# Kernel optimization log

Hardware: AMD Instinct MI355X
Metric: run time of the kernel (lower is better)

Reference implementation:

```python
import jax, jax.numpy as jnp
import numpy as np

NLAT = 192  # octahedral O96-class grid


def _lons(nlat):
    half = [20 + 4 * i for i in range(nlat // 2)]
    return half + half[::-1]


def _dft_matrix(nlat, mmax):
    # Truncated per-ring real-DFT basis (torch.fft.rfft convention, 'forward' 1/n norm).
    # Ring j has nlon_j points; frequencies beyond its Nyquist (m > nlon_j//2) are zero.
    lons = _lons(nlat)
    max_nlon = max(lons)
    D = np.zeros((nlat, max_nlon, mmax), dtype=np.complex64)
    for j, n in enumerate(lons):
        keep = min(mmax, n // 2 + 1)
        k = np.arange(n)[:, None]
        m = np.arange(keep)[None, :]
        D[j, :n, :keep] = np.exp(-2j * np.pi * k * m / n) / n
    return D


def _legendre_weights(nlat, lmax, mmax):
    # Orthonormalized associated Legendre P_l^m at Gaussian latitudes (north->south),
    # with Gaussian quadrature weights and the 2*pi longitude factor folded in.
    xg, wg = np.polynomial.legendre.leggauss(nlat)
    x = xg[::-1].copy()
    w = wg[::-1].copy()
    s = np.sqrt(1.0 - x * x)
    leg = np.zeros((lmax, mmax, nlat))
    pmm = np.full(nlat, 1.0 / np.sqrt(4.0 * np.pi))
    for m in range(mmax):
        if m > 0:
            pmm = -np.sqrt((2 * m + 1) / (2.0 * m)) * s * pmm
        if m < lmax:
            leg[m, m] = pmm
        if m + 1 < lmax:
            leg[m + 1, m] = np.sqrt(2 * m + 3.0) * x * pmm
        for l in range(m + 2, lmax):
            a = np.sqrt((4.0 * l * l - 1.0) / (l * l - m * m))
            bb = np.sqrt(((2.0 * l + 1.0) * (l - 1 + m) * (l - 1 - m)) / ((2.0 * l - 3.0) * (l * l - m * m)))
            leg[l, m] = a * x * leg[l - 1, m] - bb * leg[l - 2, m]
    leg = 2.0 * np.pi * leg * w[None, None, :]
    return leg.astype(np.float32)


def setup_inputs() -> dict:
    key = jax.random.key(0)
    nlat = NLAT
    lmax = mmax = nlat // 2
    n_points = sum(_lons(nlat))  # 40320 for nlat=192
    data = jax.random.normal(key, (4, 1, 1, n_points, 100), dtype=jnp.float32)
    dft = jnp.asarray(_dft_matrix(nlat, mmax))
    leg = jnp.asarray(_legendre_weights(nlat, lmax, mmax))
    return {"data": data, "dft": dft, "leg": leg}


def reference(data, dft, leg):
    b, t, e, p, v = data.shape
    nlat, max_nlon, mmax = dft.shape
    lmax = leg.shape[0]
    lons = _lons(nlat)
    # static scatter map: flattened ragged rings -> [nlat, max_nlon] padded layout
    flat_idx = np.concatenate([j * max_nlon + np.arange(n) for j, n in enumerate(lons)])
    x = jnp.transpose(data, (0, 1, 2, 4, 3)).reshape(-1, p)  # [(b t e v), p]
    B = x.shape[0]
    x_pad = jnp.zeros((B, nlat * max_nlon), x.dtype).at[:, flat_idx].set(x)
    x_pad = x_pad.reshape(B, nlat, max_nlon)
    # ragged per-ring truncated real DFT, then associated-Legendre contraction
    f_hat = jnp.einsum('bjn,jnm->bjm', x_pad, dft)        # [B, nlat, mmax] complex
    coeffs = jnp.einsum('bjm,lmj->blm', f_hat, leg)       # [B, lmax, mmax] complex
    coeffs = coeffs.reshape(b, t, e, v, lmax, mmax)
    return jnp.transpose(coeffs, (0, 1, 2, 4, 5, 3))      # [b, t, e, yF, xF, v]
```

## Files before the change

kernel.cpp:

```cpp
#include <hip/hip_runtime.h>

#define NLAT 192
#define NPTS 40320
#define MMAX 96
#define LMAX 96
#define NV   100
#define MAXN 400
#define NB   400

typedef __attribute__((ext_vector_type(8))) _Float16 half8v;
typedef __attribute__((ext_vector_type(4))) float f32x4;

static __device__ __forceinline__ float bits2f(unsigned int b) {
    union { unsigned int i; float f; } v; v.i = b; return v.f;
}
static __device__ __forceinline__ unsigned int f2bf(float f) {
    union { float f; unsigned int i; } v; v.f = f;
    return (v.i + 0x7FFFu + ((v.i >> 16) & 1u)) >> 16;
}
static __device__ __forceinline__ unsigned short f2h(float f) {
    union { _Float16 h; unsigned short s; } u; u.h = (_Float16)f; return u.s;
}
static __device__ __forceinline__ float h2f(unsigned short s) {
    union { _Float16 h; unsigned short s; } u; u.s = s; return (float)u.h;
}
static __device__ __forceinline__ void split2(float a, float b,
                                              unsigned int& hw, unsigned int& lw) {
    unsigned short h0 = f2h(a), h1 = f2h(b);
    unsigned short l0 = f2h(a - h2f(h0)), l1 = f2h(b - h2f(h1));
    hw = (unsigned int)h0 | ((unsigned int)h1 << 16);
    lw = (unsigned int)l0 | ((unsigned int)l1 << 16);
}

static __device__ __forceinline__ int Ssum(int n) {
    int q = n >> 3, r = n & 7; return 4 * q * (q - 1) + q * r;
}
static __device__ __forceinline__ int atoffk(int j) {
    if (j < 96) return 32 * (Ssum(j + 12) - 4);
    return 32 * (672 + 676 - Ssum(204 - j));
}
static __device__ __forceinline__ int kpad_of(int j) {
    return 32 * ((j < 96 ? (j + 12) : (203 - j)) >> 3);
}

__global__ __launch_bounds__(256) void leg_conv_kernel(
    const float* __restrict__ leg,
    unsigned short* __restrict__ legh,
    unsigned short* __restrict__ legl)
{
    int idx = blockIdx.x * 256 + threadIdx.x;
    if (idx >= 96 * 96 * 192) return;
    int j = idx % 192;
    int lm = idx / 192;
    int m = lm % 96, l = lm / 96;
    float v = leg[idx];
    unsigned short h = f2h(v);
    unsigned short lo = f2h(v - h2f(h));
    size_t o = ((size_t)m * 96 + l) * 192 + j;
    legh[o] = h;
    legl[o] = lo;
}

__global__ __launch_bounds__(256) void dft_transpose_kernel(
    const unsigned int* __restrict__ dftw,
    unsigned short* __restrict__ At)
{
    const int j = blockIdx.x;
    const int kpad = kpad_of(j);
    const int t = blockIdx.y;
    const int k0 = t * 32;
    if (k0 >= kpad) return;
    const int n = j < 96 ? 20 + 4 * j : 400 - 4 * (j - 96);
    unsigned short* abase = At + (size_t)atoffk(j) * 192 + (size_t)t * 6144;
    const int tid = threadIdx.x;
#pragma unroll
    for (int s = 0; s < 3; ++s) {
        int slot = s * 256 + tid;
        int row = slot % 192;
        int ch  = slot / 192;
        int m = row < 96 ? row : row - 96;
        bool isIm = row >= 96;
        const unsigned int* dp = dftw + ((size_t)j * MAXN + k0 + ch * 8) * 96 + m;
        unsigned short o[8];
#pragma unroll
        for (int i = 0; i < 8; ++i) {
            int k = k0 + ch * 8 + i;
            unsigned int v = (k < n) ? dp[(size_t)i * 96] : 0u;
            float f = isIm ? bits2f(v & 0xFFFF0000u) : bits2f(v << 16);
            o[i] = f2h(f);
        }
        uint4 pk;
        pk.x = (unsigned int)o[0] | ((unsigned int)o[1] << 16);
        pk.y = (unsigned int)o[2] | ((unsigned int)o[3] << 16);
        pk.z = (unsigned int)o[4] | ((unsigned int)o[5] << 16);
        pk.w = (unsigned int)o[6] | ((unsigned int)o[7] << 16);
        *(uint4*)(abase + (size_t)row * 32 + ch * 8) = pk;
    }
}

__global__ __launch_bounds__(256) void dft_mfma_kernel(
    const float* __restrict__ data,
    const unsigned short* __restrict__ At,
    unsigned short* __restrict__ fh,
    int c0, int cn)
{
    const int id  = blockIdx.x;
    const int j   = id % 192;
    const int bt  = id / 192;
    const int tid = threadIdx.x;
    const int w   = tid >> 6;
    const int l   = tid & 63;
    const int lr  = l & 15;
    const int kg  = l >> 4;

    int n, start;
    if (j < 96) { n = 20 + 4 * j; start = 2 * j * j + 18 * j; }
    else { int jj = j - 96; n = 400 - 4 * jj; start = 20160 + 402 * jj - 2 * jj * jj; }
    const int nsteps = kpad_of(j) >> 5;
    const half8v* avbase = (const half8v*)(At + (size_t)atoffk(j) * 192);

    const int Bb = c0 + bt * 50;
    const int bb = Bb / NV;
    const int vb = Bb % NV;
    const float* dbase = data + (size_t)bb * NPTS * NV + vb;

    f32x4 acc[3][4];
#pragma unroll
    for (int i = 0; i < 3; ++i)
#pragma unroll
        for (int nt = 0; nt < 4; ++nt) acc[i][nt] = (f32x4){0.f, 0.f, 0.f, 0.f};

    float xf[4][8];
#pragma unroll
    for (int nt = 0; nt < 4; ++nt) {
        int c = nt * 16 + lr;
        const float* sp = dbase + (size_t)(start + kg * 8) * NV + c;
#pragma unroll
        for (int i = 0; i < 8; ++i) {
            int k = kg * 8 + i;
            xf[nt][i] = (c < 50 && k < n) ? sp[(size_t)i * NV] : 0.f;
        }
    }

    for (int t = 0; t < nsteps; ++t) {
        const half8v* av = avbase + (size_t)t * 768;
        half8v a0 = av[((3 * w + 0) * 16 + lr) * 4 + kg];
        half8v a1 = av[((3 * w + 1) * 16 + lr) * 4 + kg];
        half8v a2 = av[((3 * w + 2) * 16 + lr) * 4 + kg];

        unsigned int BH[4][4], BL[4][4];
#pragma unroll
        for (int nt = 0; nt < 4; ++nt)
#pragma unroll
            for (int q = 0; q < 4; ++q)
                split2(xf[nt][2 * q], xf[nt][2 * q + 1], BH[nt][q], BL[nt][q]);

        if (t + 1 < nsteps) {
            int kb = (t + 1) * 32 + kg * 8;
#pragma unroll
            for (int nt = 0; nt < 4; ++nt) {
                int c = nt * 16 + lr;
                const float* sp = dbase + (size_t)(start + kb) * NV + c;
#pragma unroll
                for (int i = 0; i < 8; ++i) {
                    int k = kb + i;
                    xf[nt][i] = (c < 50 && k < n) ? sp[(size_t)i * NV] : 0.f;
                }
            }
        }

#pragma unroll
        for (int nt = 0; nt < 4; ++nt) {
            union { uint4 u; half8v h; } ub, ul2;
            ub.u = (uint4){BH[nt][0], BH[nt][1], BH[nt][2], BH[nt][3]};
            ul2.u = (uint4){BL[nt][0], BL[nt][1], BL[nt][2], BL[nt][3]};
            half8v bh = ub.h, bl = ul2.h;
            acc[0][nt] = __builtin_amdgcn_mfma_f32_16x16x32_f16(a0, bh, acc[0][nt], 0, 0, 0);
            acc[1][nt] = __builtin_amdgcn_mfma_f32_16x16x32_f16(a1, bh, acc[1][nt], 0, 0, 0);
            acc[2][nt] = __builtin_amdgcn_mfma_f32_16x16x32_f16(a2, bh, acc[2][nt], 0, 0, 0);
            acc[0][nt] = __builtin_amdgcn_mfma_f32_16x16x32_f16(a0, bl, acc[0][nt], 0, 0, 0);
            acc[1][nt] = __builtin_amdgcn_mfma_f32_16x16x32_f16(a1, bl, acc[1][nt], 0, 0, 0);
            acc[2][nt] = __builtin_amdgcn_mfma_f32_16x16x32_f16(a2, bl, acc[2][nt], 0, 0, 0);
        }
    }

#pragma unroll
    for (int i = 0; i < 3; ++i)
#pragma unroll
        for (int nt = 0; nt < 4; ++nt) {
            int c = nt * 16 + lr;
            if (c < 50) {
                int Brel = bt * 50 + c;
                int mm0 = (3 * w + i) * 16 + kg * 4;
                unsigned short* oh = fh + ((size_t)j * 192 + mm0) * cn + Brel;
#pragma unroll
                for (int r = 0; r < 4; ++r)
                    oh[(size_t)r * cn] = f2h(acc[i][nt][r]);
            }
        }
}

__global__ __launch_bounds__(256) void leg_mfma_kernel(
    const unsigned short* __restrict__ legh,
    const unsigned short* __restrict__ legl,
    const unsigned short* __restrict__ fh,
    unsigned int* __restrict__ out,
    int c0, int cn)
{
    const int m   = blockIdx.x;
    const int bt  = blockIdx.y;
    const int tid = threadIdx.x;
    const int w   = tid >> 6;
    const int l   = tid & 63;
    const int lr  = l & 15;
    const int kg  = l >> 4;

    const int c  = w * 16 + lr;
    const bool cok = c < 50;
    const int col = bt * 50 + (cok ? c : 0);

    f32x4 acc[6][2];
#pragma unroll
    for (int lt = 0; lt < 6; ++lt)
#pragma unroll
        for (int pl = 0; pl < 2; ++pl) acc[lt][pl] = (f32x4){0.f, 0.f, 0.f, 0.f};

    for (int j0 = 0; j0 < NLAT; j0 += 32) {
        half8v ah[6], al[6];
#pragma unroll
        for (int lt = 0; lt < 6; ++lt) {
            size_t o = ((size_t)m * 96 + lt * 16 + lr) * 192 + j0 + kg * 8;
            ah[lt] = *(const half8v*)&legh[o];
            al[lt] = *(const half8v*)&legl[o];
        }
        half8v fF[2];
#pragma unroll
        for (int pl = 0; pl < 2; ++pl) {
            union { half8v h; unsigned short s[8]; } uf;
#pragma unroll
            for (int i = 0; i < 8; ++i)
                uf.s[i] = fh[((size_t)(j0 + kg * 8 + i) * 192 + m + 96 * pl) * cn + col];
            fF[pl] = uf.h;
        }
#pragma unroll
        for (int lt = 0; lt < 6; ++lt)
#pragma unroll
            for (int pl = 0; pl < 2; ++pl) {
                acc[lt][pl] = __builtin_amdgcn_mfma_f32_16x16x32_f16(ah[lt], fF[pl], acc[lt][pl], 0, 0, 0);
                acc[lt][pl] = __builtin_amdgcn_mfma_f32_16x16x32_f16(al[lt], fF[pl], acc[lt][pl], 0, 0, 0);
            }
    }

    if (cok) {
        int B = c0 + bt * 50 + c;
        int bb = B / NV, vv = B % NV;
#pragma unroll
        for (int lt = 0; lt < 6; ++lt) {
#pragma unroll
            for (int r = 0; r < 4; ++r) {
                int ll = lt * 16 + kg * 4 + r;
                out[(((size_t)bb * LMAX + ll) * MMAX + m) * NV + vv] =
                    f2bf(acc[lt][0][r]) | (f2bf(acc[lt][1][r]) << 16);
            }
        }
    }
}

extern "C" void kernel_launch(void* const* d_in, const int* in_sizes, int n_in,
                              void* d_out, int out_size, void* d_ws, size_t ws_size,
                              hipStream_t stream) {
    if (n_in != 3) return;

    const float* data = (const float*)d_in[0];
    const unsigned int* dftw = (const unsigned int*)d_in[1];
    const float* leg  = (const float*)d_in[2];
    unsigned int* out = (unsigned int*)d_out;

    const size_t LEGN = (size_t)96 * 96 * 192;
    const size_t LEGB = 2 * LEGN * sizeof(unsigned short);
    const size_t ATN  = (size_t)43008 * 192;
    const size_t ATB  = ATN * sizeof(unsigned short);
    const size_t rowb = (size_t)192 * 192 * sizeof(unsigned short);
    if (ws_size < LEGB + ATB + 50 * rowb) return;

    unsigned short* legh = (unsigned short*)d_ws;
    unsigned short* legl = legh + LEGN;
    unsigned short* At   = legl + LEGN;

    size_t maxrows = (ws_size - LEGB - ATB) / rowb;
    int chunk = (int)((maxrows / 50) * 50);
    if (chunk > NB) chunk = NB;

    leg_conv_kernel<<<dim3((96 * 96 * 192 + 255) / 256), dim3(256), 0, stream>>>(
        leg, legh, legl);
    dft_transpose_kernel<<<dim3(192, 13), dim3(256), 0, stream>>>(dftw, At);

    for (int c0 = 0; c0 < NB; c0 += chunk) {
        int cn = NB - c0 < chunk ? NB - c0 : chunk;
        unsigned short* fh = At + ATN;

        int nbt = cn / 50;
        dim3 g1(192 * nbt);
        dft_mfma_kernel<<<g1, dim3(256), 0, stream>>>(data, At, fh, c0, cn);
        dim3 g2(96, nbt);
        leg_mfma_kernel<<<g2, dim3(256), 0, stream>>>(legh, legl, fh, out, c0, cn);
    }
}
```

Baseline: 96.15 us.

## Pair symmetric rings per DFT block, re-split warps, and double-buffer operand loads

The DFT kernel now has each block process a ring and its mirror ring (short plus long), so every block does the same total work and the grid shrinks by half. Warps are re-split so each wave owns one 16-column slice and all 12 m-tiles, and the next step's A fragments are prefetched through ping-pong register buffers. The Legendre kernel prefetches the next f-hat slice into registers while the current MFMAs run. The aim is to remove load imbalance across rings and hide global-load latency behind MFMA work, at the cost of more registers (24 half8 A fragments) and half as many blocks.

```diff
diff --git a/kernel.cpp b/kernel.cpp
--- a/kernel.cpp
+++ b/kernel.cpp
@@ -98,6 +98,40 @@
     }
 }
 
+static __device__ __forceinline__ void k1_step(
+    const half8v (&acur)[12], half8v (&anxt)[12], float (&xf)[8],
+    f32x4 (&acc)[12], int t, int nsteps, int n, int start, int kg,
+    int lr, bool cok, int cc, const float* __restrict__ dbase,
+    const half8v* __restrict__ avb)
+{
+    unsigned int BH[4], BL[4];
+#pragma unroll
+    for (int q = 0; q < 4; ++q)
+        split2(xf[2 * q], xf[2 * q + 1], BH[q], BL[q]);
+
+    if (t + 1 < nsteps) {
+        int kb = (t + 1) * 32 + kg * 8;
+#pragma unroll
+        for (int i = 0; i < 8; ++i) {
+            int k = kb + i;
+            xf[i] = (cok && k < n) ? dbase[(size_t)(start + k) * NV + cc] : 0.f;
+        }
+        const half8v* avn = avb + (size_t)(t + 1) * 768;
+#pragma unroll
+        for (int mt = 0; mt < 12; ++mt)
+            anxt[mt] = avn[(mt * 16 + lr) * 4 + kg];
+    }
+
+    union { uint4 u; half8v h; } ubh, ubl;
+    ubh.u = (uint4){BH[0], BH[1], BH[2], BH[3]};
+    ubl.u = (uint4){BL[0], BL[1], BL[2], BL[3]};
+#pragma unroll
+    for (int mt = 0; mt < 12; ++mt) {
+        acc[mt] = __builtin_amdgcn_mfma_f32_16x16x32_f16(acur[mt], ubh.h, acc[mt], 0, 0, 0);
+        acc[mt] = __builtin_amdgcn_mfma_f32_16x16x32_f16(acur[mt], ubl.h, acc[mt], 0, 0, 0);
+    }
+}
+
 __global__ __launch_bounds__(256) void dft_mfma_kernel(
     const float* __restrict__ data,
     const unsigned short* __restrict__ At,
@@ -105,98 +139,101 @@
     int c0, int cn)
 {
     const int id  = blockIdx.x;
-    const int j   = id % 192;
-    const int bt  = id / 192;
+    const int p   = id % 96;
+    const int bt  = id / 96;
     const int tid = threadIdx.x;
     const int w   = tid >> 6;
     const int l   = tid & 63;
     const int lr  = l & 15;
     const int kg  = l >> 4;
 
-    int n, start;
-    if (j < 96) { n = 20 + 4 * j; start = 2 * j * j + 18 * j; }
-    else { int jj = j - 96; n = 400 - 4 * jj; start = 20160 + 402 * jj - 2 * jj * jj; }
-    const int nsteps = kpad_of(j) >> 5;
-    const half8v* avbase = (const half8v*)(At + (size_t)atoffk(j) * 192);
-
     const int Bb = c0 + bt * 50;
     const int bb = Bb / NV;
     const int vb = Bb % NV;
     const float* dbase = data + (size_t)bb * NPTS * NV + vb;
-
-    f32x4 acc[3][4];
-#pragma unroll
-    for (int i = 0; i < 3; ++i)
-#pragma unroll
-        for (int nt = 0; nt < 4; ++nt) acc[i][nt] = (f32x4){0.f, 0.f, 0.f, 0.f};
-
-    float xf[4][8];
-#pragma unroll
-    for (int nt = 0; nt < 4; ++nt) {
-        int c = nt * 16 + lr;
-        const float* sp = dbase + (size_t)(start + kg * 8) * NV + c;
+    const int cc = w * 16 + lr;
+    const bool cok = cc < 50;
+
+    for (int rr = 0; rr < 2; ++rr) {
+        int j, n, start;
+        if (rr == 0) { j = p;      n = 20 + 4 * p;  start = 2 * p * p + 18 * p; }
+        else         { j = 96 + p; n = 400 - 4 * p; start = 20160 + 402 * p - 2 * p * p; }
+        const int nsteps = kpad_of(j) >> 5;
+        const half8v* avb = (const half8v*)(At + (size_t)atoffk(j) * 192);
+
+        f32x4 acc[12];
+#pragma unroll
+        for (int mt = 0; mt < 12; ++mt) acc[mt] = (f32x4){0.f, 0.f, 0.f, 0.f};
+
+        half8v aA[12], aB[12];
+        float xf[8];
+#pragma unroll
+        for (int mt = 0; mt < 12; ++mt)
+            aA[mt] = avb[(mt * 16 + lr) * 4 + kg];
 #pragma unroll
         for (int i = 0; i < 8; ++i) {
             int k = kg * 8 + i;
-            xf[nt][i] = (c < 50 && k < n) ? sp[(size_t)i * NV] : 0.f;
-        }
-    }
-
-    for (int t = 0; t < nsteps; ++t) {
-        const half8v* av = avbase + (size_t)t * 768;
-        half8v a0 = av[((3 * w + 0) * 16 + lr) * 4 + kg];
-        half8v a1 = av[((3 * w + 1) * 16 + lr) * 4 + kg];
-        half8v a2 = av[((3 * w + 2) * 16 + lr) * 4 + kg];
-
-        unsigned int BH[4][4], BL[4][4];
-#pragma unroll
-        for (int nt = 0; nt < 4; ++nt)
-#pragma unroll
-            for (int q = 0; q < 4; ++q)
-                split2(xf[nt][2 * q], xf[nt][2 * q + 1], BH[nt][q], BL[nt][q]);
-
-        if (t + 1 < nsteps) {
-            int kb = (t + 1) * 32 + kg * 8;
-#pragma unroll
-            for (int nt = 0; nt < 4; ++nt) {
-                int c = nt * 16 + lr;
-                const float* sp = dbase + (size_t)(start + kb) * NV + c;
-#pragma unroll
-                for (int i = 0; i < 8; ++i) {
-                    int k = kb + i;
-                    xf[nt][i] = (c < 50 && k < n) ? sp[(size_t)i * NV] : 0.f;
-                }
+            xf[i] = (cok && k < n) ? dbase[(size_t)(start + k) * NV + cc] : 0.f;
+        }
+
+        int t = 0;
+        while (true) {
+            k1_step(aA, aB, xf, acc, t, nsteps, n, start, kg, lr, cok, cc, dbase, avb);
+            if (++t >= nsteps) break;
+            k1_step(aB, aA, xf, acc, t, nsteps, n, start, kg, lr, cok, cc, dbase, avb);
+            if (++t >= nsteps) break;
+        }
+
+        if (cok) {
+            int Brel = bt * 50 + cc;
+#pragma unroll
+            for (int mt = 0; mt < 12; ++mt) {
+#pragma unroll
+                for (int r = 0; r < 4; ++r)
+                    fh[((size_t)j * 192 + mt * 16 + kg * 4 + r) * cn + Brel] =
+                        f2h(acc[mt][r]);
             }
         }
-
-#pragma unroll
-        for (int nt = 0; nt < 4; ++nt) {
-            union { uint4 u; half8v h; } ub, ul2;
-            ub.u = (uint4){BH[nt][0], BH[nt][1], BH[nt][2], BH[nt][3]};
-            ul2.u = (uint4){BL[nt][0], BL[nt][1], BL[nt][2], BL[nt][3]};
-            half8v bh = ub.h, bl = ul2.h;
-            acc[0][nt] = __builtin_amdgcn_mfma_f32_16x16x32_f16(a0, bh, acc[0][nt], 0, 0, 0);
-            acc[1][nt] = __builtin_amdgcn_mfma_f32_16x16x32_f16(a1, bh, acc[1][nt], 0, 0, 0);
-            acc[2][nt] = __builtin_amdgcn_mfma_f32_16x16x32_f16(a2, bh, acc[2][nt], 0, 0, 0);
-            acc[0][nt] = __builtin_amdgcn_mfma_f32_16x16x32_f16(a0, bl, acc[0][nt], 0, 0, 0);
-            acc[1][nt] = __builtin_amdgcn_mfma_f32_16x16x32_f16(a1, bl, acc[1][nt], 0, 0, 0);
-            acc[2][nt] = __builtin_amdgcn_mfma_f32_16x16x32_f16(a2, bl, acc[2][nt], 0, 0, 0);
-        }
-    }
-
-#pragma unroll
-    for (int i = 0; i < 3; ++i)
-#pragma unroll
-        for (int nt = 0; nt < 4; ++nt) {
-            int c = nt * 16 + lr;
-            if (c < 50) {
-                int Brel = bt * 50 + c;
-                int mm0 = (3 * w + i) * 16 + kg * 4;
-                unsigned short* oh = fh + ((size_t)j * 192 + mm0) * cn + Brel;
-#pragma unroll
-                for (int r = 0; r < 4; ++r)
-                    oh[(size_t)r * cn] = f2h(acc[i][nt][r]);
-            }
+    }
+}
+
+static __device__ __forceinline__ void k2_step(
+    unsigned short (&fcur)[2][8], unsigned short (&fnxt)[2][8],
+    f32x4 (&acc)[6][2], int s, int m, int lr, int kg, int col, int cn,
+    const unsigned short* __restrict__ legh,
+    const unsigned short* __restrict__ legl,
+    const unsigned short* __restrict__ fh)
+{
+    const int j0 = s * 32;
+    half8v ah[6], al[6];
+#pragma unroll
+    for (int lt = 0; lt < 6; ++lt) {
+        size_t o = ((size_t)m * 96 + lt * 16 + lr) * 192 + j0 + kg * 8;
+        ah[lt] = *(const half8v*)&legh[o];
+        al[lt] = *(const half8v*)&legl[o];
+    }
+    if (s + 1 < 6) {
+        const int jn = (s + 1) * 32 + kg * 8;
+#pragma unroll
+        for (int pl = 0; pl < 2; ++pl)
+#pragma unroll
+            for (int i = 0; i < 8; ++i)
+                fnxt[pl][i] = fh[((size_t)(jn + i) * 192 + m + 96 * pl) * cn + col];
+    }
+    half8v fF[2];
+#pragma unroll
+    for (int pl = 0; pl < 2; ++pl) {
+        union { half8v h; unsigned short s16[8]; } uf;
+#pragma unroll
+        for (int i = 0; i < 8; ++i) uf.s16[i] = fcur[pl][i];
+        fF[pl] = uf.h;
+    }
+#pragma unroll
+    for (int lt = 0; lt < 6; ++lt)
+#pragma unroll
+        for (int pl = 0; pl < 2; ++pl) {
+            acc[lt][pl] = __builtin_amdgcn_mfma_f32_16x16x32_f16(ah[lt], fF[pl], acc[lt][pl], 0, 0, 0);
+            acc[lt][pl] = __builtin_amdgcn_mfma_f32_16x16x32_f16(al[lt], fF[pl], acc[lt][pl], 0, 0, 0);
         }
 }
 
@@ -225,30 +262,17 @@
 #pragma unroll
         for (int pl = 0; pl < 2; ++pl) acc[lt][pl] = (f32x4){0.f, 0.f, 0.f, 0.f};
 
-    for (int j0 = 0; j0 < NLAT; j0 += 32) {
-        half8v ah[6], al[6];
-#pragma unroll
-        for (int lt = 0; lt < 6; ++lt) {
-            size_t o = ((size_t)m * 96 + lt * 16 + lr) * 192 + j0 + kg * 8;
-            ah[lt] = *(const half8v*)&legh[o];
-            al[lt] = *(const half8v*)&legl[o];
-        }
-        half8v fF[2];
-#pragma unroll
-        for (int pl = 0; pl < 2; ++pl) {
-            union { half8v h; unsigned short s[8]; } uf;
-#pragma unroll
-            for (int i = 0; i < 8; ++i)
-                uf.s[i] = fh[((size_t)(j0 + kg * 8 + i) * 192 + m + 96 * pl) * cn + col];
-            fF[pl] = uf.h;
-        }
-#pragma unroll
-        for (int lt = 0; lt < 6; ++lt)
-#pragma unroll
-            for (int pl = 0; pl < 2; ++pl) {
-                acc[lt][pl] = __builtin_amdgcn_mfma_f32_16x16x32_f16(ah[lt], fF[pl], acc[lt][pl], 0, 0, 0);
-                acc[lt][pl] = __builtin_amdgcn_mfma_f32_16x16x32_f16(al[lt], fF[pl], acc[lt][pl], 0, 0, 0);
-            }
+    unsigned short fA[2][8], fB[2][8];
+#pragma unroll
+    for (int pl = 0; pl < 2; ++pl)
+#pragma unroll
+        for (int i = 0; i < 8; ++i)
+            fA[pl][i] = fh[((size_t)(kg * 8 + i) * 192 + m + 96 * pl) * cn + col];
+
+#pragma unroll
+    for (int ss = 0; ss < 3; ++ss) {
+        k2_step(fA, fB, acc, 2 * ss,     m, lr, kg, col, cn, legh, legl, fh);
+        k2_step(fB, fA, acc, 2 * ss + 1, m, lr, kg, col, cn, legh, legl, fh);
     }
 
     if (cok) {
@@ -300,7 +324,7 @@
         unsigned short* fh = At + ATN;
 
         int nbt = cn / 50;
-        dim3 g1(192 * nbt);
+        dim3 g1(96 * nbt);
         dft_mfma_kernel<<<g1, dim3(256), 0, stream>>>(data, At, fh, c0, cn);
         dim3 g2(96, nbt);
         leg_mfma_kernel<<<g2, dim3(256), 0, stream>>>(legh, legl, fh, out, c0, cn);
```

After: 93.99 us. 1.02x faster.
